# Kernel tuning notes

Hardware: AMD Instinct MI355X
Metric: run time of the kernel (lower is better)

The kernel has to match this reference:

```python
import jax, jax.numpy as jnp
import numpy as np

D_MODEL = 1024
NUM_HEADS = 16
D_K = D_MODEL // NUM_HEADS
D_MLP = 4096
EPS = 1e-5


def setup_inputs() -> dict:
    key = jax.random.key(0)
    ks = jax.random.split(key, 16)
    s = 0.02
    inp = {
        "x": jax.random.normal(ks[0], (2, 2048, D_MODEL), dtype=jnp.float32),
        "Wq": jax.random.normal(ks[1], (D_MODEL, D_MODEL), dtype=jnp.float32) * s,
        "bq": jnp.zeros((D_MODEL,), jnp.float32),
        "Wk": jax.random.normal(ks[2], (D_MODEL, D_MODEL), dtype=jnp.float32) * s,
        "bk": jnp.zeros((D_MODEL,), jnp.float32),
        "Wv": jax.random.normal(ks[3], (D_MODEL, D_MODEL), dtype=jnp.float32) * s,
        "bv": jnp.zeros((D_MODEL,), jnp.float32),
        "Wo": jax.random.normal(ks[4], (D_MODEL, D_MODEL), dtype=jnp.float32) * s,
        "bo": jnp.zeros((D_MODEL,), jnp.float32),
        "W1": jax.random.normal(ks[5], (D_MODEL, D_MLP), dtype=jnp.float32) * s,
        "b1": jnp.zeros((D_MLP,), jnp.float32),
        "W2": jax.random.normal(ks[6], (D_MLP, D_MODEL), dtype=jnp.float32) * s,
        "b2": jnp.zeros((D_MODEL,), jnp.float32),
        "ln1_g": jnp.ones((D_MODEL,), jnp.float32),
        "ln1_b": jnp.zeros((D_MODEL,), jnp.float32),
        "ln2_g": jnp.ones((D_MODEL,), jnp.float32),
        "ln2_b": jnp.zeros((D_MODEL,), jnp.float32),
    }
    return inp


def _layer_norm(x, g, b):
    mu = jnp.mean(x, axis=-1, keepdims=True)
    var = jnp.var(x, axis=-1, keepdims=True)
    return (x - mu) * jax.lax.rsqrt(var + EPS) * g + b


def _split_heads(x):
    b, s, _ = x.shape
    return x.reshape(b, s, NUM_HEADS, D_K).transpose(0, 2, 1, 3)  # [b,h,s,dk]


def reference(x, Wq, bq, Wk, bk, Wv, bv, Wo, bo, W1, b1, W2, b2,
              ln1_g, ln1_b, ln2_g, ln2_b):
    b, s, _ = x.shape
    q = _split_heads(x @ Wq + bq)
    k = _split_heads(x @ Wk + bk)
    v = _split_heads(x @ Wv + bv)
    # [b,h,s,s] scores, scaled by sqrt(d_k) as in the original
    score = jnp.einsum("bhqd,bhkd->bhqk", q, k) / jnp.sqrt(jnp.float32(D_K))
    attn = jax.nn.softmax(score, axis=-1)
    out = jnp.einsum("bhqk,bhkd->bhqd", attn, v)
    out = out.transpose(0, 2, 1, 3).reshape(b, s, D_MODEL)
    out = out @ Wo + bo
    # residual + norm1 (dropout is identity in eval)
    x = _layer_norm(x + out, ln1_g, ln1_b)
    # feed-forward
    h = jax.nn.relu(x @ W1 + b1)
    ff = h @ W2 + b2
    x = _layer_norm(x + ff, ln2_g, ln2_b)
    return x
```

## Files before the change

kernel.cpp:

```cpp
#include <hip/hip_runtime.h>
#include <hip/hip_bf16.h>
#include <cstdint>

#define DEV __device__ __forceinline__

typedef __attribute__((ext_vector_type(8))) __bf16 bf16x8;
typedef __attribute__((ext_vector_type(4))) float f32x4;

DEV uint16_t f2b(float f) {
  __hip_bfloat16 h = __float2bfloat16(f);
  return *(uint16_t*)&h;
}
DEV uint32_t pkbf2(float a, float b) {
  return (uint32_t)f2b(a) | ((uint32_t)f2b(b) << 16);
}

DEV void gload_lds16(const void* g, void* l) {
  __builtin_amdgcn_global_load_lds(
      (const __attribute__((address_space(1))) void*)g,
      (__attribute__((address_space(3))) void*)l, 16, 0, 0);
}

DEV bf16x8 scale8(bf16x8 v, float sc) {
  union { bf16x8 b; uint16_t u[8]; } in, out;
  in.b = v;
#pragma unroll
  for (int i = 0; i < 8; i++) {
    float x = __uint_as_float(((uint32_t)in.u[i]) << 16);
    out.u[i] = f2b(x * sc);
  }
  return out.b;
}

__global__ __launch_bounds__(256) void prep_all(
    const float* __restrict__ x, uint16_t* __restrict__ xb,
    const float* __restrict__ Wq, const float* __restrict__ Wk,
    const float* __restrict__ Wv, uint16_t* __restrict__ wqkt,
    const float* __restrict__ Wo, uint16_t* __restrict__ wot,
    const float* __restrict__ W1, uint16_t* __restrict__ w1t,
    const float* __restrict__ W2, uint16_t* __restrict__ w2t,
    const float* __restrict__ bq, const float* __restrict__ bk,
    const float* __restrict__ bv, float* __restrict__ bqkv) {
  __shared__ float t[32][33];
  int bid = blockIdx.x, tid = threadIdx.x;
  if (bid < 4096) {
    int i = bid * 256 + tid;
    float4 v = ((const float4*)x)[i];
    uint2 r;
    r.x = pkbf2(v.x, v.y);
    r.y = pkbf2(v.z, v.w);
    ((uint2*)xb)[i] = r;
    return;
  }
  if (bid >= 16384) {
    int i = (bid - 16384) * 256 + tid;
    if (i < 3072)
      bqkv[i] = i < 1024 ? bq[i] : (i < 2048 ? bk[i - 1024] : bv[i - 2048]);
    return;
  }
  const float* src;
  uint16_t* dst;
  int R, C, bx, by;
  if (bid < 8192) {
    int local = bid - 4096;
    if (local < 3072) {
      int z = local >> 10, rem = local & 1023;
      src = z == 0 ? Wq : (z == 1 ? Wk : Wv);
      dst = wqkt + (size_t)z * 1024 * 1024;
      R = 1024; C = 1024; bx = rem & 31; by = rem >> 5;
    } else {
      int rem = local - 3072;
      src = Wo; dst = wot; R = 1024; C = 1024; bx = rem & 31; by = rem >> 5;
    }
  } else if (bid < 12288) {
    int rem = bid - 8192;
    src = W1; dst = w1t; R = 1024; C = 4096; bx = rem & 127; by = rem >> 7;
  } else {
    int rem = bid - 12288;
    src = W2; dst = w2t; R = 4096; C = 1024; bx = rem & 31; by = rem >> 5;
  }
  int c0 = bx * 32, r0 = by * 32;
  int tx = tid & 31, ty = tid >> 5;
#pragma unroll
  for (int i = 0; i < 4; i++)
    t[ty + 8 * i][tx] = src[(size_t)(r0 + ty + 8 * i) * C + c0 + tx];
  __syncthreads();
#pragma unroll
  for (int i = 0; i < 4; i++)
    dst[(size_t)(c0 + ty + 8 * i) * R + r0 + tx] = f2b(t[tx][ty + 8 * i]);
}

__global__ __launch_bounds__(256) void transpose_v(
    const uint16_t* __restrict__ qkv, uint16_t* __restrict__ Vt) {
  __shared__ uint16_t t[32][33];
  int bh = blockIdx.z, b = bh >> 4, h = bh & 15;
  int s0 = blockIdx.x * 32, d0 = blockIdx.y * 32;
  int tx = threadIdx.x & 31, ty = threadIdx.x >> 5;
#pragma unroll
  for (int i = 0; i < 4; i++)
    t[ty + 8 * i][tx] =
        qkv[(size_t)(b * 2048 + s0 + ty + 8 * i) * 3072 + 2048 + h * 64 + d0 + tx];
  __syncthreads();
#pragma unroll
  for (int i = 0; i < 4; i++)
    Vt[((size_t)bh * 64 + d0 + ty + 8 * i) * 2048 + s0 + tx] = t[tx][ty + 8 * i];
}

template <int MODE, int NSPLIT, int BK>
__global__ __launch_bounds__(256) void gemm_bt(
    const uint16_t* __restrict__ A, const uint16_t* __restrict__ Bt,
    const float* __restrict__ bias, void* __restrict__ Cv,
    int M, int N, int K, int nx) {
  __shared__ uint16_t As[2][128 * BK];
  __shared__ uint16_t Bs[2][128 * BK];
  int nwg = gridDim.x, bid = blockIdx.x;
  int cpx = nwg >> 3;
  int swzb = (bid & 7) * cpx + (bid >> 3);
  int ntile = nwg / NSPLIT;
  int sp = swzb / ntile, r = swzb % ntile;
  int n0 = (r % nx) * 128, m0 = (r / nx) * 128;
  int Klen = K / NSPLIT;
  int tid = threadIdx.x, w = tid >> 6, l = tid & 63;
  int wr = w >> 1, wc = w & 1;
  int lr = l & 15, lg = l >> 4, lk8 = lg * 8;
  f32x4 acc[4][4] = {};
  const uint16_t* Ab = A + (size_t)m0 * K + sp * Klen;
  const uint16_t* Bb = Bt + (size_t)n0 * K + sp * Klen;

  auto stage = [&](int buf, int k0) {
    if (BK == 32) {
#pragma unroll
      for (int i = 0; i < 2; i++) {
        int c = 2 * w + i;
        int rr = c * 16 + (l >> 2);
        gload_lds16(Ab + (size_t)rr * K + k0 + (l & 3) * 8, &As[buf][c * 512]);
        gload_lds16(Bb + (size_t)rr * K + k0 + (l & 3) * 8, &Bs[buf][c * 512]);
      }
    } else {
      int colb = (((l & 7) ^ ((l >> 3) & 7)) << 4);
#pragma unroll
      for (int i = 0; i < 4; i++) {
        int c = 4 * w + i;
        int rr = c * 8 + (l >> 3);
        gload_lds16((const uint8_t*)(Ab + (size_t)rr * K + k0) + colb,
                    &As[buf][c * 512]);
        gload_lds16((const uint8_t*)(Bb + (size_t)rr * K + k0) + colb,
                    &Bs[buf][c * 512]);
      }
    }
  };

  stage(0, 0);
  __syncthreads();

  for (int k0 = 0; k0 < Klen; k0 += BK) {
    int cur = (k0 / BK) & 1;
    if (k0 + BK < Klen) stage(cur ^ 1, k0 + BK);
    if (BK == 32) {
      bf16x8 af[4], bf[4];
#pragma unroll
      for (int m = 0; m < 4; m++)
        af[m] = *(const bf16x8*)&As[cur][(wr * 64 + m * 16 + lr) * 32 + lk8];
#pragma unroll
      for (int n = 0; n < 4; n++)
        bf[n] = *(const bf16x8*)&Bs[cur][(wc * 64 + n * 16 + lr) * 32 + lk8];
#pragma unroll
      for (int m = 0; m < 4; m++)
#pragma unroll
        for (int n = 0; n < 4; n++)
          acc[m][n] = __builtin_amdgcn_mfma_f32_16x16x32_bf16(af[m], bf[n], acc[m][n], 0, 0, 0);
    } else {
      int sw = (lr & 7) << 4;
#pragma unroll
      for (int ks = 0; ks < 2; ks++) {
        int off = ((ks << 6) | (lg << 4)) ^ sw;
        bf16x8 af[4], bf[4];
#pragma unroll
        for (int m = 0; m < 4; m++)
          af[m] = *(const bf16x8*)((const uint8_t*)&As[cur][(wr * 64 + m * 16 + lr) * 64] + off);
#pragma unroll
        for (int n = 0; n < 4; n++)
          bf[n] = *(const bf16x8*)((const uint8_t*)&Bs[cur][(wc * 64 + n * 16 + lr) * 64] + off);
#pragma unroll
        for (int m = 0; m < 4; m++)
#pragma unroll
          for (int n = 0; n < 4; n++)
            acc[m][n] = __builtin_amdgcn_mfma_f32_16x16x32_bf16(af[m], bf[n], acc[m][n], 0, 0, 0);
      }
    }
    __syncthreads();
  }

  int g4 = lg * 4;
#pragma unroll
  for (int m = 0; m < 4; m++) {
    int row = m0 + wr * 64 + m * 16 + g4;
#pragma unroll
    for (int n = 0; n < 4; n++) {
      int col = n0 + wc * 64 + n * 16 + lr;
      float bv = (NSPLIT == 1 || sp == 0) ? bias[col] : 0.f;
#pragma unroll
      for (int j = 0; j < 4; j++) {
        float v = acc[m][n][j] + bv;
        if (MODE == 2) v = fmaxf(v, 0.f);
        size_t idx = (size_t)sp * M * N + (size_t)(row + j) * N + col;
        if (MODE == 0) ((float*)Cv)[idx] = v;
        else           ((uint16_t*)Cv)[idx] = f2b(v);
      }
    }
  }
}

template <int MODE, int NSPLIT>
__global__ __launch_bounds__(512, 2) void gemm256(
    const uint16_t* __restrict__ A, const uint16_t* __restrict__ Bt,
    const float* __restrict__ bias, void* __restrict__ Cv,
    int M, int N, int K, int nx) {
  __shared__ uint16_t As[2][256 * 64];
  __shared__ uint16_t Bs[2][256 * 64];
  int nwg = gridDim.x, bid = blockIdx.x;
  int cpx = nwg >> 3;
  int swzb = (bid & 7) * cpx + (bid >> 3);
  int ntile = nwg / NSPLIT;
  int sp = swzb / ntile, rr0 = swzb % ntile;
  int n0 = (rr0 % nx) * 256, m0 = (rr0 / nx) * 256;
  int Klen = K / NSPLIT;
  int tid = threadIdx.x, w = tid >> 6, l = tid & 63;
  int wr = w >> 2, wc = w & 3;
  int lr = l & 15, lg = l >> 4;
  f32x4 acc[8][4] = {};
  const uint16_t* Ab = A + (size_t)m0 * K + sp * Klen;
  const uint16_t* Bb = Bt + (size_t)n0 * K + sp * Klen;
  int colb = (((l & 7) ^ (l >> 3)) << 4);
  int srl = l >> 3;

  auto stageH = [&](int buf, int k0, int h) {
    const uint16_t* base = (h < 2) ? Ab : Bb;
    uint16_t* lds = (h < 2) ? &As[buf][0] : &Bs[buf][0];
    int hh = (h & 1) * 128;
#pragma unroll
    for (int j = 0; j < 2; j++) {
      int rr = hh + j * 64 + w * 8;
      gload_lds16((const uint8_t*)(base + (size_t)(rr + srl) * K + k0) + colb,
                  &lds[rr * 64]);
    }
  };

#pragma unroll
  for (int h = 0; h < 4; h++) stageH(0, 0, h);
  asm volatile("s_waitcnt vmcnt(0)" ::: "memory");
  __builtin_amdgcn_s_barrier();

  int nt = Klen >> 6;
  int swr = (lr & 7) << 4;
  for (int t = 0; t < nt; t++) {
    int buf = t & 1;
    bf16x8 bfr[2][4];
#pragma unroll
    for (int ks = 0; ks < 2; ks++) {
#pragma unroll
      for (int mq = 0; mq < 2; mq++) {
        const int ph = ks * 2 + mq;
        int off = ((ks << 6) | (lg << 4)) ^ swr;
        bf16x8 af[4];
#pragma unroll
        for (int m = 0; m < 4; m++) {
          int row = wr * 128 + (mq * 4 + m) * 16 + lr;
          af[m] = *(const bf16x8*)((const uint8_t*)&As[buf][row * 64] + off);
        }
        if (mq == 0) {
#pragma unroll
          for (int n = 0; n < 4; n++) {
            int row = wc * 64 + n * 16 + lr;
            bfr[ks][n] = *(const bf16x8*)((const uint8_t*)&Bs[buf][row * 64] + off);
          }
        }
        if (t + 1 < nt) {
          if (ph == 0) { stageH(buf ^ 1, (t + 1) * 64, 0); stageH(buf ^ 1, (t + 1) * 64, 1); }
          if (ph == 1) { stageH(buf ^ 1, (t + 1) * 64, 2); stageH(buf ^ 1, (t + 1) * 64, 3); }
        }
        __builtin_amdgcn_s_barrier();
        asm volatile("s_waitcnt lgkmcnt(0)" ::: "memory");
        __builtin_amdgcn_sched_barrier(0);
        __builtin_amdgcn_s_setprio(1);
#pragma unroll
        for (int m = 0; m < 4; m++)
#pragma unroll
          for (int n = 0; n < 4; n++)
            acc[mq * 4 + m][n] = __builtin_amdgcn_mfma_f32_16x16x32_bf16(
                af[m], bfr[ks][n], acc[mq * 4 + m][n], 0, 0, 0);
        __builtin_amdgcn_s_setprio(0);
        if (ph == 3) asm volatile("s_waitcnt vmcnt(0)" ::: "memory");
        __builtin_amdgcn_s_barrier();
      }
    }
  }

#pragma unroll
  for (int m = 0; m < 8; m++) {
    int row = m0 + wr * 128 + m * 16 + lg * 4;
#pragma unroll
    for (int n = 0; n < 4; n++) {
      int col = n0 + wc * 64 + n * 16 + lr;
      float bv = (NSPLIT == 1 || sp == 0) ? bias[col] : 0.f;
#pragma unroll
      for (int j = 0; j < 4; j++) {
        float v = acc[m][n][j] + bv;
        if (MODE == 2) v = fmaxf(v, 0.f);
        size_t idx = (size_t)sp * M * N + (size_t)(row + j) * N + col;
        if (MODE == 0) ((float*)Cv)[idx] = v;
        else           ((uint16_t*)Cv)[idx] = f2b(v);
      }
    }
  }
}

__global__ __launch_bounds__(256, 2) void attn_fused(
    const uint16_t* __restrict__ qkv, const uint16_t* __restrict__ Vt,
    uint16_t* __restrict__ outb) {
  constexpr int LQ = 3072;
  constexpr float SC = 0.18033688f;
  int L = blockIdx.x;
  int qb = (L >> 3) & 15;
  int bh = (L & 7) + 8 * (L >> 7);
  int b = bh >> 4, h = bh & 15;
  int w = threadIdx.x >> 6, l = threadIdx.x & 63;
  int lr = l & 15, lg = l >> 4;
  int qbase = qb * 128 + w * 32;

  __shared__ uint16_t Kbuf[2][2][64 * 64];
  __shared__ uint16_t Vbuf[2][2][64 * 64];
  __shared__ uint16_t Plds[4][2][16 * 64];
  uint16_t* PwA = &Plds[w][0][0];
  uint16_t* PwB = &Plds[w][1][0];

  const uint16_t* qrowA = qkv + (size_t)(b * 2048 + qbase + lr) * LQ + h * 64;
  const uint16_t* qrowB = qrowA + (size_t)16 * LQ;
  bf16x8 qA0 = scale8(*(const bf16x8*)(qrowA + lg * 8), SC);
  bf16x8 qA1 = scale8(*(const bf16x8*)(qrowA + 32 + lg * 8), SC);
  bf16x8 qB0 = scale8(*(const bf16x8*)(qrowB + lg * 8), SC);
  bf16x8 qB1 = scale8(*(const bf16x8*)(qrowB + 32 + lg * 8), SC);

  float rsA = 0.f, rsB = 0.f;
  f32x4 oA[4] = {}, oB[4] = {};

  const uint8_t* kq = (const uint8_t*)qkv;
  const uint8_t* vq = (const uint8_t*)Vt;
  int colb = (((l & 7) ^ ((l >> 3) & 7)) << 4);
  int Rl = w * 16 + (l >> 3);

  auto stageKV = [&](int buf, int kb) {
#pragma unroll
    for (int s2 = 0; s2 < 2; s2++) {
#pragma unroll
      for (int c2 = 0; c2 < 2; c2++) {
        int R = Rl + c2 * 8;
        const uint8_t* ks =
            kq + ((size_t)(b * 2048 + kb + s2 * 64 + R) * LQ + 1024 + h * 64) * 2 + colb;
        gload_lds16(ks, &Kbuf[buf][s2][(w * 16 + c2 * 8) * 64]);
        const uint8_t* vs =
            vq + ((size_t)(bh * 64 + R) * 2048 + kb + s2 * 64) * 2 + colb;
        gload_lds16(vs, &Vbuf[buf][s2][(w * 16 + c2 * 8) * 64]);
      }
    }
  };

  stageKV(0, 0);
  __syncthreads();

  int swz = (lr & 7) << 4;
  for (int kb = 0; kb < 2048; kb += 128) {
    int cur = (kb >> 7) & 1;
    if (kb + 128 < 2048) stageKV(cur ^ 1, kb + 128);

#pragma unroll
    for (int s2 = 0; s2 < 2; s2++) {
      const uint8_t* Kb = (const uint8_t*)Kbuf[cur][s2];
      const uint8_t* Vb = (const uint8_t*)Vbuf[cur][s2];
      f32x4 sA[4], sB[4];
      __builtin_amdgcn_s_setprio(1);
#pragma unroll
      for (int t = 0; t < 4; t++) {
        const uint8_t* rb = Kb + (16 * t + lr) * 128;
        bf16x8 k0 = *(const bf16x8*)(rb + ((lg << 4) ^ swz));
        bf16x8 k1 = *(const bf16x8*)(rb + ((64 | (lg << 4)) ^ swz));
        f32x4 zA = {};
        zA = __builtin_amdgcn_mfma_f32_16x16x32_bf16(k0, qA0, zA, 0, 0, 0);
        zA = __builtin_amdgcn_mfma_f32_16x16x32_bf16(k1, qA1, zA, 0, 0, 0);
        sA[t] = zA;
        f32x4 zB = {};
        zB = __builtin_amdgcn_mfma_f32_16x16x32_bf16(k0, qB0, zB, 0, 0, 0);
        zB = __builtin_amdgcn_mfma_f32_16x16x32_bf16(k1, qB1, zB, 0, 0, 0);
        sB[t] = zB;
      }
      __builtin_amdgcn_s_setprio(0);
#pragma unroll
      for (int t = 0; t < 4; t++) {
        float a0 = __builtin_amdgcn_exp2f(sA[t][0]);
        float a1 = __builtin_amdgcn_exp2f(sA[t][1]);
        float a2 = __builtin_amdgcn_exp2f(sA[t][2]);
        float a3 = __builtin_amdgcn_exp2f(sA[t][3]);
        rsA += (a0 + a1) + (a2 + a3);
        uint2 pa;
        pa.x = pkbf2(a0, a1);
        pa.y = pkbf2(a2, a3);
        *(uint2*)((uint8_t*)PwA + lr * 128 + ((t * 32 + lg * 8) ^ swz)) = pa;
        float b0 = __builtin_amdgcn_exp2f(sB[t][0]);
        float b1 = __builtin_amdgcn_exp2f(sB[t][1]);
        float b2 = __builtin_amdgcn_exp2f(sB[t][2]);
        float b3 = __builtin_amdgcn_exp2f(sB[t][3]);
        rsB += (b0 + b1) + (b2 + b3);
        uint2 pb;
        pb.x = pkbf2(b0, b1);
        pb.y = pkbf2(b2, b3);
        *(uint2*)((uint8_t*)PwB + lr * 128 + ((t * 32 + lg * 8) ^ swz)) = pb;
      }
      __builtin_amdgcn_wave_barrier();
      bf16x8 pA0 = *(const bf16x8*)((const uint8_t*)PwA + lr * 128 + ((lg << 4) ^ swz));
      bf16x8 pA1 = *(const bf16x8*)((const uint8_t*)PwA + lr * 128 + ((64 | (lg << 4)) ^ swz));
      bf16x8 pB0 = *(const bf16x8*)((const uint8_t*)PwB + lr * 128 + ((lg << 4) ^ swz));
      bf16x8 pB1 = *(const bf16x8*)((const uint8_t*)PwB + lr * 128 + ((64 | (lg << 4)) ^ swz));
      __builtin_amdgcn_s_setprio(1);
#pragma unroll
      for (int t = 0; t < 4; t++) {
        const uint8_t* rb = Vb + (16 * t + lr) * 128;
        bf16x8 v0 = *(const bf16x8*)(rb + ((lg << 4) ^ swz));
        bf16x8 v1 = *(const bf16x8*)(rb + ((64 | (lg << 4)) ^ swz));
        oA[t] = __builtin_amdgcn_mfma_f32_16x16x32_bf16(v0, pA0, oA[t], 0, 0, 0);
        oA[t] = __builtin_amdgcn_mfma_f32_16x16x32_bf16(v1, pA1, oA[t], 0, 0, 0);
        oB[t] = __builtin_amdgcn_mfma_f32_16x16x32_bf16(v0, pB0, oB[t], 0, 0, 0);
        oB[t] = __builtin_amdgcn_mfma_f32_16x16x32_bf16(v1, pB1, oB[t], 0, 0, 0);
      }
      __builtin_amdgcn_s_setprio(0);
      if (s2 == 0) __builtin_amdgcn_wave_barrier();
    }
    __syncthreads();
  }
  rsA += __shfl_xor(rsA, 16);
  rsA += __shfl_xor(rsA, 32);
  rsB += __shfl_xor(rsB, 16);
  rsB += __shfl_xor(rsB, 32);
  float invA = 1.f / rsA, invB = 1.f / rsB;
  uint16_t* orowA = outb + (size_t)(b * 2048 + qbase + lr) * 1024 + h * 64;
  uint16_t* orowB = orowA + (size_t)16 * 1024;
#pragma unroll
  for (int t = 0; t < 4; t++) {
    uint2 ra;
    ra.x = pkbf2(oA[t][0] * invA, oA[t][1] * invA);
    ra.y = pkbf2(oA[t][2] * invA, oA[t][3] * invA);
    *(uint2*)(orowA + t * 16 + lg * 4) = ra;
    uint2 rb2;
    rb2.x = pkbf2(oB[t][0] * invB, oB[t][1] * invB);
    rb2.y = pkbf2(oB[t][2] * invB, oB[t][3] * invB);
    *(uint2*)(orowB + t * 16 + lg * 4) = rb2;
  }
}

template <int XBF, int WF32, int WB16, int NPART>
__global__ __launch_bounds__(256) void ln_res(
    const void* __restrict__ xr, const uint16_t* __restrict__ parts,
    const float* __restrict__ gam, const float* __restrict__ bet,
    float* __restrict__ of32, uint16_t* __restrict__ ob16) {
  int row = blockIdx.x, t = threadIdx.x;
  int w = t >> 6, l = t & 63;
  float v0, v1, v2, v3;
  if (XBF) {
    uint2 u = ((const uint2*)((const uint16_t*)xr + (size_t)row * 1024))[t];
    v0 = __uint_as_float((u.x & 0xffffu) << 16);
    v1 = __uint_as_float(u.x & 0xffff0000u);
    v2 = __uint_as_float((u.y & 0xffffu) << 16);
    v3 = __uint_as_float(u.y & 0xffff0000u);
  } else {
    float4 xv = ((const float4*)((const float*)xr + (size_t)row * 1024))[t];
    v0 = xv.x; v1 = xv.y; v2 = xv.z; v3 = xv.w;
  }
#pragma unroll
  for (int p = 0; p < NPART; p++) {
    uint2 u = ((const uint2*)(parts + (size_t)p * 4096 * 1024 +
                              (size_t)row * 1024))[t];
    v0 += __uint_as_float((u.x & 0xffffu) << 16);
    v1 += __uint_as_float(u.x & 0xffff0000u);
    v2 += __uint_as_float((u.y & 0xffffu) << 16);
    v3 += __uint_as_float(u.y & 0xffff0000u);
  }
  float s = v0 + v1 + v2 + v3;
  float sq = v0 * v0 + v1 * v1 + v2 * v2 + v3 * v3;
#pragma unroll
  for (int d = 1; d < 64; d <<= 1) {
    s += __shfl_xor(s, d);
    sq += __shfl_xor(sq, d);
  }
  __shared__ float red[8];
  if (l == 0) { red[w] = s; red[4 + w] = sq; }
  __syncthreads();
  s = red[0] + red[1] + red[2] + red[3];
  sq = red[4] + red[5] + red[6] + red[7];
  float mean = s * (1.f / 1024.f);
  float var = sq * (1.f / 1024.f) - mean * mean;
  float rstd = rsqrtf(var + 1e-5f);
  float4 gv = ((const float4*)gam)[t];
  float4 bv = ((const float4*)bet)[t];
  float y0 = (v0 - mean) * rstd * gv.x + bv.x;
  float y1 = (v1 - mean) * rstd * gv.y + bv.y;
  float y2 = (v2 - mean) * rstd * gv.z + bv.z;
  float y3 = (v3 - mean) * rstd * gv.w + bv.w;
  if (WF32) {
    float4 yv; yv.x = y0; yv.y = y1; yv.z = y2; yv.w = y3;
    ((float4*)(of32 + (size_t)row * 1024))[t] = yv;
  }
  if (WB16) {
    uint2 r;
    r.x = pkbf2(y0, y1);
    r.y = pkbf2(y2, y3);
    ((uint2*)(ob16 + (size_t)row * 1024))[t] = r;
  }
}

static constexpr size_t OFF_XB    = 0;
static constexpr size_t OFF_WQKVT = (size_t)8 << 20;
static constexpr size_t OFF_WOT   = (size_t)14 << 20;
static constexpr size_t OFF_W1T   = (size_t)16 << 20;
static constexpr size_t OFF_W2T   = (size_t)24 << 20;
static constexpr size_t OFF_BIAS  = (size_t)32 << 20;
static constexpr size_t OFF_QKV   = OFF_BIAS + ((size_t)64 << 10);
static constexpr size_t OFF_VT    = OFF_QKV + ((size_t)24 << 20);
static constexpr size_t OFF_PROJ  = OFF_VT + ((size_t)8 << 20);
static constexpr size_t OFF_LN1B  = OFF_PROJ + ((size_t)32 << 20);

extern "C" void kernel_launch(void* const* d_in, const int* in_sizes, int n_in,
                              void* d_out, int out_size, void* d_ws, size_t ws_size,
                              hipStream_t stream) {
  const float* x   = (const float*)d_in[0];
  const float* Wq  = (const float*)d_in[1];
  const float* bq  = (const float*)d_in[2];
  const float* Wk  = (const float*)d_in[3];
  const float* bk  = (const float*)d_in[4];
  const float* Wv  = (const float*)d_in[5];
  const float* bv  = (const float*)d_in[6];
  const float* Wo  = (const float*)d_in[7];
  const float* bo  = (const float*)d_in[8];
  const float* W1  = (const float*)d_in[9];
  const float* b1  = (const float*)d_in[10];
  const float* W2  = (const float*)d_in[11];
  const float* b2  = (const float*)d_in[12];
  const float* g1  = (const float*)d_in[13];
  const float* be1 = (const float*)d_in[14];
  const float* g2  = (const float*)d_in[15];
  const float* be2 = (const float*)d_in[16];
  float* out = (float*)d_out;
  uint8_t* ws = (uint8_t*)d_ws;

  uint16_t* xb    = (uint16_t*)(ws + OFF_XB);
  uint16_t* wqkt  = (uint16_t*)(ws + OFF_WQKVT);
  uint16_t* wot   = (uint16_t*)(ws + OFF_WOT);
  uint16_t* w1t   = (uint16_t*)(ws + OFF_W1T);
  uint16_t* w2t   = (uint16_t*)(ws + OFF_W2T);
  float*    bqkv  = (float*)(ws + OFF_BIAS);
  uint16_t* qkvb  = (uint16_t*)(ws + OFF_QKV);
  uint16_t* vt    = (uint16_t*)(ws + OFF_VT);
  uint16_t* proj  = (uint16_t*)(ws + OFF_PROJ);
  uint16_t* ln1b  = (uint16_t*)(ws + OFF_LN1B);
  uint16_t* attnb = (uint16_t*)(ws + OFF_XB);
  uint16_t* hbuf  = (uint16_t*)(ws + OFF_QKV);

  prep_all<<<16396, 256, 0, stream>>>(x, xb, Wq, Wk, Wv, wqkt, Wo, wot,
                                      W1, w1t, W2, w2t, bq, bk, bv, bqkv);
  gemm_bt<1, 1, 32><<<768, 256, 0, stream>>>(xb, wqkt, bqkv, qkvb,
                                             4096, 3072, 1024, 24);
  transpose_v<<<dim3(64, 2, 32), 256, 0, stream>>>(qkvb, vt);
  attn_fused<<<512, 256, 0, stream>>>(qkvb, vt, attnb);
  gemm_bt<1, 2, 64><<<512, 256, 0, stream>>>(attnb, wot, bo, proj,
                                             4096, 1024, 1024, 8);
  ln_res<0, 0, 1, 2><<<4096, 256, 0, stream>>>(x, proj, g1, be1,
                                               nullptr, ln1b);
  gemm256<2, 1><<<256, 512, 0, stream>>>(ln1b, w1t, b1, hbuf,
                                         4096, 4096, 1024, 16);
  gemm256<1, 4><<<256, 512, 0, stream>>>(hbuf, w2t, b2, proj,
                                         4096, 1024, 4096, 4);
  ln_res<1, 1, 0, 4><<<4096, 256, 0, stream>>>(ln1b, proj, g2, be2,
                                               out, nullptr);
}
```

Baseline: 211.1 us.

## Vectorize transposes, use 256-tile GEMM for out-proj, bf16 residual

Rewrites the weight and V transpose kernels so each thread loads a 4-element vector and stores a packed 64-bit bf16 result instead of scalar 2-byte accesses. The output projection now runs on the gemm256 kernel with a 4-way K split instead of gemm_bt with a 2-way split. The first LayerNorm reads the bf16 copy of x, which means attention output needs its own workspace buffer. This cuts global memory transactions and launch overheads, but the bf16 residual drops some precision and the split-K partial layout changes.

After: 217.6 us. 3.1% more time.

```diff
diff --git a/kernel.cpp b/kernel.cpp
--- a/kernel.cpp
+++ b/kernel.cpp
@@ -13,6 +13,9 @@
 }
 DEV uint32_t pkbf2(float a, float b) {
   return (uint32_t)f2b(a) | ((uint32_t)f2b(b) << 16);
+}
+DEV uint64_t pkbf4(float a, float b, float c, float d) {
+  return (uint64_t)pkbf2(a, b) | ((uint64_t)pkbf2(c, d) << 32);
 }
 
 DEV void gload_lds16(const void* g, void* l) {
@@ -46,10 +49,7 @@
   if (bid < 4096) {
     int i = bid * 256 + tid;
     float4 v = ((const float4*)x)[i];
-    uint2 r;
-    r.x = pkbf2(v.x, v.y);
-    r.y = pkbf2(v.z, v.w);
-    ((uint2*)xb)[i] = r;
+    ((uint64_t*)xb)[i] = pkbf4(v.x, v.y, v.z, v.w);
     return;
   }
   if (bid >= 16384) {
@@ -80,14 +80,14 @@
     src = W2; dst = w2t; R = 4096; C = 1024; bx = rem & 31; by = rem >> 5;
   }
   int c0 = bx * 32, r0 = by * 32;
-  int tx = tid & 31, ty = tid >> 5;
-#pragma unroll
-  for (int i = 0; i < 4; i++)
-    t[ty + 8 * i][tx] = src[(size_t)(r0 + ty + 8 * i) * C + c0 + tx];
+  int lrow = tid >> 3, lc = (tid & 7) * 4;
+  float4 v = *(const float4*)&src[(size_t)(r0 + lrow) * C + c0 + lc];
+  t[lrow][lc] = v.x; t[lrow][lc + 1] = v.y;
+  t[lrow][lc + 2] = v.z; t[lrow][lc + 3] = v.w;
   __syncthreads();
-#pragma unroll
-  for (int i = 0; i < 4; i++)
-    dst[(size_t)(c0 + ty + 8 * i) * R + r0 + tx] = f2b(t[tx][ty + 8 * i]);
+  int cr = tid >> 3, rq = (tid & 7) * 4;
+  uint64_t r = pkbf4(t[rq][cr], t[rq + 1][cr], t[rq + 2][cr], t[rq + 3][cr]);
+  *(uint64_t*)&dst[(size_t)(c0 + cr) * R + r0 + rq] = r;
 }
 
 __global__ __launch_bounds__(256) void transpose_v(
@@ -95,15 +95,19 @@
   __shared__ uint16_t t[32][33];
   int bh = blockIdx.z, b = bh >> 4, h = bh & 15;
   int s0 = blockIdx.x * 32, d0 = blockIdx.y * 32;
-  int tx = threadIdx.x & 31, ty = threadIdx.x >> 5;
-#pragma unroll
-  for (int i = 0; i < 4; i++)
-    t[ty + 8 * i][tx] =
-        qkv[(size_t)(b * 2048 + s0 + ty + 8 * i) * 3072 + 2048 + h * 64 + d0 + tx];
+  int tid = threadIdx.x;
+  int lrow = tid >> 3, lc = (tid & 7) * 4;
+  uint64_t v = *(const uint64_t*)&qkv[(size_t)(b * 2048 + s0 + lrow) * 3072 +
+                                      2048 + h * 64 + d0 + lc];
+  t[lrow][lc] = (uint16_t)v;
+  t[lrow][lc + 1] = (uint16_t)(v >> 16);
+  t[lrow][lc + 2] = (uint16_t)(v >> 32);
+  t[lrow][lc + 3] = (uint16_t)(v >> 48);
   __syncthreads();
-#pragma unroll
-  for (int i = 0; i < 4; i++)
-    Vt[((size_t)bh * 64 + d0 + ty + 8 * i) * 2048 + s0 + tx] = t[tx][ty + 8 * i];
+  int cr = tid >> 3, rq = (tid & 7) * 4;
+  uint64_t r = (uint64_t)t[rq][cr] | ((uint64_t)t[rq + 1][cr] << 16) |
+               ((uint64_t)t[rq + 2][cr] << 32) | ((uint64_t)t[rq + 3][cr] << 48);
+  *(uint64_t*)&Vt[((size_t)bh * 64 + d0 + cr) * 2048 + s0 + rq] = r;
 }
 
 template <int MODE, int NSPLIT, int BK>
@@ -526,6 +530,7 @@
 static constexpr size_t OFF_VT    = OFF_QKV + ((size_t)24 << 20);
 static constexpr size_t OFF_PROJ  = OFF_VT + ((size_t)8 << 20);
 static constexpr size_t OFF_LN1B  = OFF_PROJ + ((size_t)32 << 20);
+static constexpr size_t OFF_ATTN  = OFF_LN1B + ((size_t)8 << 20);
 
 extern "C" void kernel_launch(void* const* d_in, const int* in_sizes, int n_in,
                               void* d_out, int out_size, void* d_ws, size_t ws_size,
@@ -560,7 +565,7 @@
   uint16_t* vt    = (uint16_t*)(ws + OFF_VT);
   uint16_t* proj  = (uint16_t*)(ws + OFF_PROJ);
   uint16_t* ln1b  = (uint16_t*)(ws + OFF_LN1B);
-  uint16_t* attnb = (uint16_t*)(ws + OFF_XB);
+  uint16_t* attnb = (uint16_t*)(ws + OFF_ATTN);
   uint16_t* hbuf  = (uint16_t*)(ws + OFF_QKV);
 
   prep_all<<<16396, 256, 0, stream>>>(x, xb, Wq, Wk, Wv, wqkt, Wo, wot,
@@ -569,9 +574,9 @@
                                              4096, 3072, 1024, 24);
   transpose_v<<<dim3(64, 2, 32), 256, 0, stream>>>(qkvb, vt);
   attn_fused<<<512, 256, 0, stream>>>(qkvb, vt, attnb);
-  gemm_bt<1, 2, 64><<<512, 256, 0, stream>>>(attnb, wot, bo, proj,
-                                             4096, 1024, 1024, 8);
-  ln_res<0, 0, 1, 2><<<4096, 256, 0, stream>>>(x, proj, g1, be1,
+  gemm256<1, 4><<<256, 512, 0, stream>>>(attnb, wot, bo, proj,
+                                         4096, 1024, 1024, 4);
+  ln_res<1, 0, 1, 4><<<4096, 256, 0, stream>>>(xb, proj, g1, be1,
                                                nullptr, ln1b);
   gemm256<2, 1><<<256, 512, 0, stream>>>(ln1b, w1t, b1, hbuf,
                                          4096, 4096, 1024, 16);
```
